# Performance work log

Hardware: AMD Instinct MI355X
Metric: run time of the kernel (lower is better)

The kernel has to match this reference:

```python
import jax, jax.numpy as jnp
import numpy as np

K_EDE = 10.0  # IR-Net EDE k
T_EDE = 0.1   # IR-Net EDE t

@jax.custom_vjp
def binquant(x):
    # forward: sign; backward: EDE STE k*t*(1 - tanh(t*x)^2)
    return jnp.sign(x)

def _bq_fwd(x):
    return jnp.sign(x), x

def _bq_bwd(x, g):
    t = jnp.tanh(x * T_EDE)
    return (K_EDE * T_EDE * (1.0 - t * t) * g,)

binquant.defvjp(_bq_fwd, _bq_bwd)

def irconv2d(x, w, stride, groups):
    # IRConv2d: per-out-channel standardize weights, sign-binarize weights
    # and activations, rescale by detached power-of-two scale, then conv.
    oc = w.shape[0]
    wf = w.reshape(oc, -1)
    mean = jnp.mean(wf, axis=-1)[:, None, None, None]
    std = jnp.std(wf, axis=-1, ddof=1)[:, None, None, None]  # torch unbiased std
    bw = (w - mean) / std
    scale = 2.0 ** jnp.round(jnp.log2(jnp.mean(jnp.abs(bw).reshape(oc, -1), axis=-1)))
    sw = jax.lax.stop_gradient(scale)[:, None, None, None]
    bw = binquant(bw) * sw
    ba = binquant(x)
    return jax.lax.conv_general_dilated(
        ba, bw, window_strides=(stride, stride), padding=((1, 1), (1, 1)),
        dimension_numbers=("NCHW", "OIHW", "NCHW"), feature_group_count=groups)

def batchnorm(x, gamma, beta, mean, var, eps=1e-5):
    inv = gamma / jnp.sqrt(var + eps)
    return x * inv[None, :, None, None] + (beta - mean * inv)[None, :, None, None]

def setup_inputs() -> dict:
    key = jax.random.key(0)
    ks = jax.random.split(key, 8)
    B, C, H, W, G = 64, 256, 28, 28, 4
    x = jax.random.normal(ks[0], (B, C, H, W), dtype=jnp.float32)
    w1 = jax.random.normal(ks[1], (G, C, C // G, 3, 3), dtype=jnp.float32) * 0.05
    g1 = jnp.ones((G, C), dtype=jnp.float32)
    b1 = jnp.zeros((G, C), dtype=jnp.float32)
    m1 = jax.random.normal(ks[2], (G, C), dtype=jnp.float32) * 0.1
    v1 = jax.random.uniform(ks[3], (G, C), dtype=jnp.float32, minval=0.5, maxval=1.5)
    w2 = jax.random.normal(ks[4], (C, C, 3, 3), dtype=jnp.float32) * 0.05
    g2 = jnp.ones((C,), dtype=jnp.float32)
    b2 = jnp.zeros((C,), dtype=jnp.float32)
    m2 = jax.random.normal(ks[5], (C,), dtype=jnp.float32) * 0.1
    v2 = jax.random.uniform(ks[6], (C,), dtype=jnp.float32, minval=0.5, maxval=1.5)
    return {"x": x, "w1": w1, "g1": g1, "b1": b1, "m1": m1, "v1": v1,
            "w2": w2, "g2": g2, "b2": b2, "m2": m2, "v2": v2}

def reference(x, w1, g1, b1, m1, v1, w2, g2, b2, m2, v2):
    groups = w1.shape[0]
    identity = x  # downsample is None
    x_max = jax.lax.stop_gradient(jnp.max(jnp.abs(x)))
    out = jnp.zeros_like(x)
    for i in range(groups):
        alpha = -1.0 + (i + 1) * 2.0 / (groups + 1)
        xi = x + alpha * x_max
        yi = irconv2d(xi, w1[i], stride=1, groups=groups)
        yi = batchnorm(yi, g1[i], b1[i], m1[i], v1[i])
        out = out + yi
    out = out + identity
    out = jnp.clip(out, -1.0, 1.0)  # Hardtanh
    identity = out
    out = irconv2d(out, w2, stride=1, groups=1)
    out = batchnorm(out, g2, b2, m2, v2)
    out = out + identity
    return jnp.clip(out, -1.0, 1.0)
```

## Files before the change

### kernel.cpp

```cpp
#include <hip/hip_runtime.h>
#include <stdint.h>

typedef uint32_t u32; typedef uint64_t u64; typedef unsigned short u16;

#define NB   64
#define NC   256
#define NG   4
#define HW   784
#define PHW  900
#define NTOT 12845056

#define OFF_XMAX 0
#define OFF_FLG1 64
#define OFF_FLG2 1088
#define OFF_W1P  2048
#define OFF_W2P  75776
#define OFF_A1   149504
#define OFF_S1   153600
#define OFF_A2   157696
#define OFF_S2   158720
#define OFF_C1   159744
#define OFF_C2   196608
#define OFF_BA1  205824
#define OFF_BZ1  7578624
#define OFF_BA2  14951424
#define OFF_BZ2  16794624

__device__ inline double wredsumd(double v) {
#pragma unroll
    for (int off = 32; off; off >>= 1) v += __shfl_xor(v, off);
    return v;
}

__global__ __launch_bounds__(256) void k_absmax(const float4* __restrict__ x, u32* __restrict__ xmax, int n4) {
    u32 m = 0;
    int idx = blockIdx.x * blockDim.x + threadIdx.x;
    int stride = gridDim.x * blockDim.x;
    for (int i = idx; i < n4; i += stride) {
        float4 v = x[i];
        m = max(m, __float_as_uint(v.x) & 0x7fffffffu);
        m = max(m, __float_as_uint(v.y) & 0x7fffffffu);
        m = max(m, __float_as_uint(v.z) & 0x7fffffffu);
        m = max(m, __float_as_uint(v.w) & 0x7fffffffu);
    }
#pragma unroll
    for (int off = 32; off; off >>= 1) {
        u32 o = (u32)__shfl_xor((int)m, off);
        m = max(m, o);
    }
    __shared__ u32 sm[4];
    int lane = threadIdx.x & 63, wid = threadIdx.x >> 6;
    if (lane == 0) sm[wid] = m;
    __syncthreads();
    if (threadIdx.x == 0) {
        u32 mm = max(max(sm[0], sm[1]), max(sm[2], sm[3]));
        atomicMax(xmax, mm);
    }
}

__global__ __launch_bounds__(256) void k_prep1(const float* __restrict__ w1, const float* __restrict__ g1,
                                               const float* __restrict__ b1, const float* __restrict__ m1,
                                               const float* __restrict__ v1, char* __restrict__ ws) {
    int lane = threadIdx.x & 63, wid = threadIdx.x >> 6;
    int cc = blockIdx.x * 4 + wid;
    int i = cc >> 8, oc = cc & 255;
    const float* wp = w1 + ((size_t)(i * 256 + oc) * 64 + lane) * 9;
    float v[9];
#pragma unroll
    for (int t = 0; t < 9; t++) v[t] = wp[t];
    double s = 0.0;
#pragma unroll
    for (int t = 0; t < 9; t++) s += (double)v[t];
    s = wredsumd(s);
    double mean = s / 576.0;
    double ssq = 0.0, sab = 0.0;
#pragma unroll
    for (int t = 0; t < 9; t++) { double d = (double)v[t] - mean; ssq += d * d; sab += fabs(d); }
    ssq = wredsumd(ssq); sab = wredsumd(sab);
    double stdv = sqrt(ssq / 575.0);
    double meanabs = sab / 576.0 / stdv;
    float scale = (float)exp2(rint(log2(meanabs)));
    int bi = i * 256 + oc;
    float inv = __fdiv_rn(g1[bi], __fsqrt_rn(__fadd_rn(v1[bi], 1e-5f)));
    float A = __fmul_rn(scale, inv);
    float S = __fsub_rn(b1[bi], __fmul_rn(m1[bi], inv));

    u64* w1p = (u64*)(ws + OFF_W1P);
    int c[9]; u64 keep = 0;
#pragma unroll
    for (int t = 0; t < 9; t++) {
        u64 bal = __ballot((double)v[t] > mean);
        c[t] = 64 - 2 * (int)__popcll(bal);
        if (lane == t) keep = bal;
    }
    if (lane < 9) w1p[(size_t)(oc * 4 + i) * 9 + lane] = keep;
    if (lane == 0) {
        ((float*)(ws + OFF_A1))[oc * 4 + i] = A;
        ((float*)(ws + OFF_S1))[oc * 4 + i] = S;
        float* C1 = (float*)(ws + OFF_C1);
#pragma unroll
        for (int pat = 0; pat < 9; pat++) {
            int rt = pat / 3, ct = pat % 3, corr = 0;
#pragma unroll
            for (int t = 0; t < 9; t++) {
                int dh = t / 3 - 1, dw = t % 3 - 1;
                bool inval = (rt == 0 && dh < 0) || (rt == 2 && dh > 0) || (ct == 0 && dw < 0) || (ct == 2 && dw > 0);
                if (inval) corr += c[t];
            }
            C1[(oc * 4 + i) * 9 + pat] = (float)(576 - corr);
        }
    }
}

__global__ __launch_bounds__(256) void k_prep2(const float* __restrict__ w2, const float* __restrict__ g2,
                                               const float* __restrict__ b2, const float* __restrict__ m2,
                                               const float* __restrict__ v2, char* __restrict__ ws) {
    int lane = threadIdx.x & 63, wid = threadIdx.x >> 6;
    int oc = blockIdx.x * 4 + wid;
    float v[36];
#pragma unroll
    for (int icw = 0; icw < 4; icw++)
#pragma unroll
        for (int t = 0; t < 9; t++)
            v[icw * 9 + t] = w2[(size_t)(oc * 256 + icw * 64 + lane) * 9 + t];
    double s = 0.0;
#pragma unroll
    for (int k = 0; k < 36; k++) s += (double)v[k];
    s = wredsumd(s);
    double mean = s / 2304.0;
    double ssq = 0.0, sab = 0.0;
#pragma unroll
    for (int k = 0; k < 36; k++) { double d = (double)v[k] - mean; ssq += d * d; sab += fabs(d); }
    ssq = wredsumd(ssq); sab = wredsumd(sab);
    double stdv = sqrt(ssq / 2303.0);
    double meanabs = sab / 2304.0 / stdv;
    float scale = (float)exp2(rint(log2(meanabs)));
    float inv = __fdiv_rn(g2[oc], __fsqrt_rn(__fadd_rn(v2[oc], 1e-5f)));
    float A = __fmul_rn(scale, inv);
    float S = __fsub_rn(b2[oc], __fmul_rn(m2[oc], inv));

    u64* w2p = (u64*)(ws + OFF_W2P);
    int c2[9] = {0,0,0,0,0,0,0,0,0};
    u64 keep = 0;
#pragma unroll
    for (int icw = 0; icw < 4; icw++)
#pragma unroll
        for (int t = 0; t < 9; t++) {
            u64 bal = __ballot((double)v[icw * 9 + t] > mean);
            c2[t] += 64 - 2 * (int)__popcll(bal);
            if (lane == t * 4 + icw) keep = bal;
        }
    if (lane < 36) w2p[(size_t)oc * 36 + lane] = keep;
    if (lane == 0) {
        ((float*)(ws + OFF_A2))[oc] = A;
        ((float*)(ws + OFF_S2))[oc] = S;
        float* C2 = (float*)(ws + OFF_C2);
#pragma unroll
        for (int pat = 0; pat < 9; pat++) {
            int rt = pat / 3, ct = pat % 3, corr = 0;
#pragma unroll
            for (int t = 0; t < 9; t++) {
                int dh = t / 3 - 1, dw = t % 3 - 1;
                bool inval = (rt == 0 && dh < 0) || (rt == 2 && dh > 0) || (ct == 0 && dw < 0) || (ct == 2 && dw > 0);
                if (inval) corr += c2[t];
            }
            C2[oc * 9 + pat] = (float)(2304 - corr);
        }
    }
}

__global__ __launch_bounds__(256) void k_pack(const float* __restrict__ x, char* __restrict__ ws) {
    int g = blockIdx.x / 225, bb = blockIdx.x % 225;
    int fp = bb * 256 + threadIdx.x;
    int n = fp / 900, idx = fp - n * 900;
    int ph = idx / 30, pw = idx - ph * 30;
    u64* ba1 = (u64*)(ws + OFF_BA1);
    u64* bz1 = (u64*)(ws + OFF_BZ1);
    bool halo = (ph == 0) | (ph == 29) | (pw == 0) | (pw == 29);
    if (halo) {
#pragma unroll
        for (int i = 0; i < 4; i++) {
            size_t o = (size_t)((i * 64 + n) * 4 + g) * 900 + idx;
            ba1[o] = 0; bz1[o] = 0;
        }
        ((u64*)(ws + OFF_BA2))[(size_t)(n * 4 + g) * 900 + idx] = 0;
        ((u64*)(ws + OFF_BZ2))[(size_t)(n * 4 + g) * 900 + idx] = 0;
        return;
    }
    float xmax = *(const float*)(ws + OFF_XMAX);
    float t0 = __fmul_rn(-0.6f, xmax), t1 = __fmul_rn(-0.2f, xmax);
    float t2 = __fmul_rn(0.2f, xmax), t3 = __fmul_rn(0.6f, xmax);
    int h = ph - 1, w = pw - 1;
    const float* xb = x + (size_t)(n * 256 + g * 64) * 784 + (h * 28 + w);
    u64 wd0 = 0, wd1 = 0, wd2 = 0, wd3 = 0;
    u64 zd0 = 0, zd1 = 0, zd2 = 0, zd3 = 0;
#pragma unroll 8
    for (int c = 0; c < 64; c++) {
        float v = xb[(size_t)c * 784];
        float s0 = __fadd_rn(v, t0), s1 = __fadd_rn(v, t1);
        float s2 = __fadd_rn(v, t2), s3 = __fadd_rn(v, t3);
        wd0 |= (u64)(s0 > 0.f) << c;  zd0 |= (u64)(s0 == 0.f) << c;
        wd1 |= (u64)(s1 > 0.f) << c;  zd1 |= (u64)(s1 == 0.f) << c;
        wd2 |= (u64)(s2 > 0.f) << c;  zd2 |= (u64)(s2 == 0.f) << c;
        wd3 |= (u64)(s3 > 0.f) << c;  zd3 |= (u64)(s3 == 0.f) << c;
    }
    ba1[(size_t)((0 * 64 + n) * 4 + g) * 900 + idx] = wd0;
    ba1[(size_t)((1 * 64 + n) * 4 + g) * 900 + idx] = wd1;
    ba1[(size_t)((2 * 64 + n) * 4 + g) * 900 + idx] = wd2;
    ba1[(size_t)((3 * 64 + n) * 4 + g) * 900 + idx] = wd3;
    bz1[(size_t)((0 * 64 + n) * 4 + g) * 900 + idx] = zd0;
    bz1[(size_t)((1 * 64 + n) * 4 + g) * 900 + idx] = zd1;
    bz1[(size_t)((2 * 64 + n) * 4 + g) * 900 + idx] = zd2;
    bz1[(size_t)((3 * 64 + n) * 4 + g) * 900 + idx] = zd3;
    if (zd0 | zd1 | zd2 | zd3) atomicOr((u32*)(ws + OFF_FLG1) + (n * 4 + g), 1u);
}

__global__ __launch_bounds__(256) void k_conv1(const float* __restrict__ x, float* __restrict__ out,
                                               char* __restrict__ ws) {
    int gq = blockIdx.x / 196, bb = blockIdx.x % 196;
    int g = gq >> 2, q = gq & 3;
    int fp = bb * 256 + threadIdx.x;
    int n = fp / 784, pos = fp - n * 784;
    int h = pos / 28, w = pos - h * 28;
    int rt = (h == 0) ? 0 : ((h == 27) ? 2 : 1);
    int ct = (w == 0) ? 0 : ((w == 27) ? 2 : 1);
    int pat = rt * 3 + ct;
    int pb = (h + 1) * 30 + (w + 1);

    __shared__ u64   wsm[576];
    __shared__ float c1s[576];
    {
        const u64* wsrc = (const u64*)(ws + OFF_W1P) + (size_t)g * 2304 + q * 576;
        const float* C1 = (const float*)(ws + OFF_C1) + g * 2304 + q * 576;
        for (int k = threadIdx.x; k < 576; k += 256) { wsm[k] = wsrc[k]; c1s[k] = C1[k]; }
    }
    const u64* ba1 = (const u64*)(ws + OFF_BA1);
    u64 aw[4][9];
#pragma unroll
    for (int i = 0; i < 4; i++) {
        const u64* bp = ba1 + (size_t)((i * 64 + n) * 4 + g) * 900 + pb;
#pragma unroll
        for (int t = 0; t < 9; t++) { int dh = t / 3 - 1, dw = t % 3 - 1; aw[i][t] = bp[dh * 30 + dw]; }
    }
    u32 zflag = ((const u32*)(ws + OFF_FLG1))[n * 4 + g];
    __syncthreads();

    const float* A1 = (const float*)(ws + OFF_A1) + g * 256 + q * 64;
    const float* S1 = (const float*)(ws + OFF_S1) + g * 256 + q * 64;
    const float* xb = x + (size_t)(n * 256 + g * 64 + q * 16) * 784 + pos;
    float* ob = out + (size_t)(n * 256 + g * 64 + q * 16) * 784 + pos;
    u32 bits = 0, zbits = 0;
    if (!zflag) {
        float id[16];
#pragma unroll
        for (int j = 0; j < 16; j++) id[j] = xb[(size_t)j * 784];
#pragma unroll
        for (int j = 0; j < 16; j++) {
            const u64* wp = wsm + j * 36;
            u32 D[4];
#pragma unroll
            for (int i = 0; i < 4; i++) {
                u32 d = 0;
#pragma unroll
                for (int t = 0; t < 9; t++) d += (u32)__popcll(aw[i][t] ^ wp[i * 9 + t]);
                D[i] = d;
            }
            float acc = 0.f;
#pragma unroll
            for (int i = 0; i < 4; i++) {
                float cf = c1s[(j * 4 + i) * 9 + pat];
                float conv = __fmaf_rn(-2.f, (float)D[i], cf);
                float yi = __fadd_rn(__fmul_rn(conv, A1[j * 4 + i]), S1[j * 4 + i]);
                acc = (i == 0) ? yi : __fadd_rn(acc, yi);
            }
            float o = __fadd_rn(acc, id[j]);
            o = fminf(fmaxf(o, -1.f), 1.f);
            bits  |= (u32)(o > 0.f) << j;
            zbits |= (u32)(o == 0.f) << j;
            ob[(size_t)j * 784] = o;
        }
    } else {
        const u64* bz1 = (const u64*)(ws + OFF_BZ1);
        for (int j = 0; j < 16; j++) {
            const u64* wp = wsm + j * 36;
            float acc = 0.f;
#pragma unroll
            for (int i = 0; i < 4; i++) {
                const u64* zp = bz1 + (size_t)((i * 64 + n) * 4 + g) * 900 + pb;
                u32 d = 0; int cz = 0;
#pragma unroll
                for (int t = 0; t < 9; t++) {
                    int dh = t / 3 - 1, dw = t % 3 - 1;
                    u64 zt = zp[dh * 30 + dw];
                    d += (u32)__popcll(aw[i][t] ^ wp[i * 9 + t]);
                    cz += 2 * (int)__popcll(zt & wp[i * 9 + t]) - (int)__popcll(zt);
                }
                float cf = c1s[(j * 4 + i) * 9 + pat];
                float conv = __fadd_rn(__fmaf_rn(-2.f, (float)d, cf), (float)cz);
                float yi = __fadd_rn(__fmul_rn(conv, A1[j * 4 + i]), S1[j * 4 + i]);
                acc = (i == 0) ? yi : __fadd_rn(acc, yi);
            }
            float o = __fadd_rn(acc, xb[(size_t)j * 784]);
            o = fminf(fmaxf(o, -1.f), 1.f);
            bits  |= (u32)(o > 0.f) << j;
            zbits |= (u32)(o == 0.f) << j;
            ob[(size_t)j * 784] = o;
        }
    }
    size_t widx = (size_t)(n * 4 + g) * 900 + pb;
    ((u16*)(ws + OFF_BA2))[widx * 4 + q] = (u16)bits;
    ((u16*)(ws + OFF_BZ2))[widx * 4 + q] = (u16)zbits;
    if (zbits) atomicOr((u32*)(ws + OFF_FLG2) + n, 1u);
}

__global__ __launch_bounds__(256) void k_conv2(float* __restrict__ out, char* __restrict__ ws) {
    int tq = blockIdx.x / 196, bb = blockIdx.x % 196;
    int oq = tq >> 2, q = tq & 3;
    int fp = bb * 256 + threadIdx.x;
    int n = fp / 784, pos = fp - n * 784;
    int h = pos / 28, w = pos - h * 28;
    int rt = (h == 0) ? 0 : ((h == 27) ? 2 : 1);
    int ct = (w == 0) ? 0 : ((w == 27) ? 2 : 1);
    int pat = rt * 3 + ct;
    int pb = (h + 1) * 30 + (w + 1);

    __shared__ u64   wsm[576];
    __shared__ float c2s[144];
    {
        const u64* wsrc = (const u64*)(ws + OFF_W2P) + (size_t)(oq * 64 + q * 16) * 36;
        for (int k = threadIdx.x; k < 576; k += 256) wsm[k] = wsrc[k];
        const float* C2 = (const float*)(ws + OFF_C2) + (oq * 64 + q * 16) * 9;
        if (threadIdx.x < 144) c2s[threadIdx.x] = C2[threadIdx.x];
    }
    const u64* ba2 = (const u64*)(ws + OFF_BA2);
    u64 aw[4][9];
#pragma unroll
    for (int icw = 0; icw < 4; icw++) {
        const u64* bp = ba2 + (size_t)(n * 4 + icw) * 900 + pb;
#pragma unroll
        for (int t = 0; t < 9; t++) { int dh = t / 3 - 1, dw = t % 3 - 1; aw[icw][t] = bp[dh * 30 + dw]; }
    }
    u32 zflag = ((const u32*)(ws + OFF_FLG2))[n];
    __syncthreads();

    const float* A2 = (const float*)(ws + OFF_A2) + oq * 64 + q * 16;
    const float* S2 = (const float*)(ws + OFF_S2) + oq * 64 + q * 16;
    float* ob = out + ((size_t)n * 256 + oq * 64 + q * 16) * 784 + pos;
    if (!zflag) {
        float id[16];
#pragma unroll
        for (int j = 0; j < 16; j++) id[j] = ob[(size_t)j * 784];
#pragma unroll
        for (int j = 0; j < 16; j++) {
            const u64* wp = wsm + j * 36;
            u32 dp0 = 0, dp1 = 0, dp2 = 0, dp3 = 0;
#pragma unroll
            for (int t = 0; t < 9; t++) {
                dp0 += (u32)__popcll(aw[0][t] ^ wp[t * 4 + 0]);
                dp1 += (u32)__popcll(aw[1][t] ^ wp[t * 4 + 1]);
                dp2 += (u32)__popcll(aw[2][t] ^ wp[t * 4 + 2]);
                dp3 += (u32)__popcll(aw[3][t] ^ wp[t * 4 + 3]);
            }
            u32 d = (dp0 + dp1) + (dp2 + dp3);
            float cf = c2s[j * 9 + pat];
            float conv = __fmaf_rn(-2.f, (float)d, cf);
            float y = __fadd_rn(__fmul_rn(conv, A2[j]), S2[j]);
            float o = __fadd_rn(y, id[j]);
            o = fminf(fmaxf(o, -1.f), 1.f);
            ob[(size_t)j * 784] = o;
        }
    } else {
        const u64* bz2 = (const u64*)(ws + OFF_BZ2);
        for (int j = 0; j < 16; j++) {
            const u64* wp = wsm + j * 36;
            u32 d = 0; int cz = 0;
#pragma unroll
            for (int icw = 0; icw < 4; icw++) {
                const u64* zp = bz2 + (size_t)(n * 4 + icw) * 900 + pb;
#pragma unroll
                for (int t = 0; t < 9; t++) {
                    int dh = t / 3 - 1, dw = t % 3 - 1;
                    u64 zt = zp[dh * 30 + dw];
                    d += (u32)__popcll(aw[icw][t] ^ wp[t * 4 + icw]);
                    cz += 2 * (int)__popcll(zt & wp[t * 4 + icw]) - (int)__popcll(zt);
                }
            }
            float cf = c2s[j * 9 + pat];
            float conv = __fadd_rn(__fmaf_rn(-2.f, (float)d, cf), (float)cz);
            float y = __fadd_rn(__fmul_rn(conv, A2[j]), S2[j]);
            float idf = ob[(size_t)j * 784];
            float o = __fadd_rn(y, idf);
            o = fminf(fmaxf(o, -1.f), 1.f);
            ob[(size_t)j * 784] = o;
        }
    }
}

extern "C" void kernel_launch(void* const* d_in, const int* in_sizes, int n_in,
                              void* d_out, int out_size, void* d_ws, size_t ws_size,
                              hipStream_t stream) {
    const float* x  = (const float*)d_in[0];
    const float* w1 = (const float*)d_in[1];
    const float* g1 = (const float*)d_in[2];
    const float* b1 = (const float*)d_in[3];
    const float* m1 = (const float*)d_in[4];
    const float* v1 = (const float*)d_in[5];
    const float* w2 = (const float*)d_in[6];
    const float* g2 = (const float*)d_in[7];
    const float* b2 = (const float*)d_in[8];
    const float* m2 = (const float*)d_in[9];
    const float* v2 = (const float*)d_in[10];
    float* out = (float*)d_out;
    char* ws = (char*)d_ws;

    hipMemsetAsync(ws, 0, 2048, stream);
    k_absmax<<<512, 256, 0, stream>>>((const float4*)x, (u32*)(ws + OFF_XMAX), NTOT / 4);
    k_prep1<<<256, 256, 0, stream>>>(w1, g1, b1, m1, v1, ws);
    k_prep2<<<64, 256, 0, stream>>>(w2, g2, b2, m2, v2, ws);
    k_pack<<<900, 256, 0, stream>>>(x, ws);
    k_conv1<<<3136, 256, 0, stream>>>(x, out, ws);
    k_conv2<<<3136, 256, 0, stream>>>(out, ws);
}
```

Measured before the change: 322.4 us.

## Replace popcount binary convs with FP8 MFMA implicit-GEMM path

Adds a new path that encodes the sign-binarized weights and activations as FP8 values (+1/-1/0) in MFMA-friendly tiled layouts and runs both convolutions as implicit GEMMs with 32x32x16 fp8 MFMA instructions. Zero padding is a literal halo of zeros, so the per-pattern border correction tables and zero-flag branches are no longer needed. The path runs only when the workspace is large enough, and falls back to the old XOR/popcount kernels otherwise. It uses a much larger workspace (byte-per-element activations) and depends on the FP8 accumulation giving exact integer sums.

```diff
diff --git a/kernel.cpp b/kernel.cpp
--- a/kernel.cpp
+++ b/kernel.cpp
@@ -2,12 +2,9 @@
 #include <stdint.h>
 
 typedef uint32_t u32; typedef uint64_t u64; typedef unsigned short u16;
-
-#define NB   64
-#define NC   256
-#define NG   4
-#define HW   784
-#define PHW  900
+typedef long long i64;
+typedef float v16f __attribute__((ext_vector_type(16)));
+
 #define NTOT 12845056
 
 #define OFF_XMAX 0
@@ -26,6 +23,14 @@
 #define OFF_BA2  14951424
 #define OFF_BZ2  16794624
 
+#define MOFF_AS1   64
+#define MOFF_AS2   8256
+#define MOFF_W1F   16384
+#define MOFF_W2F   606208
+#define MOFF_ACT1  1196032
+#define MOFF_ACT2  60182528
+#define MNEED      74940416ULL
+
 __device__ inline double wredsumd(double v) {
 #pragma unroll
     for (int off = 32; off; off >>= 1) v += __shfl_xor(v, off);
@@ -58,9 +63,10 @@
     }
 }
 
-__global__ __launch_bounds__(256) void k_prep1(const float* __restrict__ w1, const float* __restrict__ g1,
-                                               const float* __restrict__ b1, const float* __restrict__ m1,
-                                               const float* __restrict__ v1, char* __restrict__ ws) {
+
+__global__ __launch_bounds__(256) void k_prep1m(const float* __restrict__ w1, const float* __restrict__ g1,
+                                                const float* __restrict__ b1, const float* __restrict__ m1,
+                                                const float* __restrict__ v1, char* __restrict__ ws) {
     int lane = threadIdx.x & 63, wid = threadIdx.x >> 6;
     int cc = blockIdx.x * 4 + wid;
     int i = cc >> 8, oc = cc & 255;
@@ -85,36 +91,25 @@
     float A = __fmul_rn(scale, inv);
     float S = __fsub_rn(b1[bi], __fmul_rn(m1[bi], inv));
 
-    u64* w1p = (u64*)(ws + OFF_W1P);
-    int c[9]; u64 keep = 0;
+    unsigned char* w1f = (unsigned char*)(ws + MOFF_W1F);
+    int g = oc >> 6, oc64 = oc & 63, ocb = oc64 >> 5, oc32 = oc64 & 31;
+    size_t blk0 = ((size_t)(((g * 4 + i) * 2 + ocb) * 18)) << 10;
 #pragma unroll
     for (int t = 0; t < 9; t++) {
-        u64 bal = __ballot((double)v[t] > mean);
-        c[t] = 64 - 2 * (int)__popcll(bal);
-        if (lane == t) keep = bal;
-    }
-    if (lane < 9) w1p[(size_t)(oc * 4 + i) * 9 + lane] = keep;
-    if (lane == 0) {
-        ((float*)(ws + OFF_A1))[oc * 4 + i] = A;
-        ((float*)(ws + OFF_S1))[oc * 4 + i] = S;
-        float* C1 = (float*)(ws + OFF_C1);
-#pragma unroll
-        for (int pat = 0; pat < 9; pat++) {
-            int rt = pat / 3, ct = pat % 3, corr = 0;
-#pragma unroll
-            for (int t = 0; t < 9; t++) {
-                int dh = t / 3 - 1, dw = t % 3 - 1;
-                bool inval = (rt == 0 && dh < 0) || (rt == 2 && dh > 0) || (ct == 0 && dw < 0) || (ct == 2 && dw > 0);
-                if (inval) corr += c[t];
-            }
-            C1[(oc * 4 + i) * 9 + pat] = (float)(576 - corr);
-        }
-    }
-}
-
-__global__ __launch_bounds__(256) void k_prep2(const float* __restrict__ w2, const float* __restrict__ g2,
-                                               const float* __restrict__ b2, const float* __restrict__ m2,
-                                               const float* __restrict__ v2, char* __restrict__ ws) {
+        int k = t * 64 + lane;
+        int kb = k >> 4;
+        size_t off = blk0 + ((size_t)(kb >> 1) << 10)
+                   + (size_t)((((k >> 3) & 1) * 32 + oc32) * 16 + (kb & 1) * 8 + (k & 7));
+        double dv = (double)v[t];
+        w1f[off] = (dv > mean) ? 0x38 : ((dv < mean) ? 0xB8 : 0x00);
+    }
+    if (lane == 0)
+        ((float2*)(ws + MOFF_AS1))[(g * 4 + i) * 64 + oc64] = make_float2(A, S);
+}
+
+__global__ __launch_bounds__(256) void k_prep2m(const float* __restrict__ w2, const float* __restrict__ g2,
+                                                const float* __restrict__ b2, const float* __restrict__ m2,
+                                                const float* __restrict__ v2, char* __restrict__ ws) {
     int lane = threadIdx.x & 63, wid = threadIdx.x >> 6;
     int oc = blockIdx.x * 4 + wid;
     float v[36];
@@ -139,6 +134,257 @@
     float A = __fmul_rn(scale, inv);
     float S = __fsub_rn(b2[oc], __fmul_rn(m2[oc], inv));
 
+    unsigned char* w2f = (unsigned char*)(ws + MOFF_W2F);
+    int ocb = oc >> 5, oc32 = oc & 31;
+#pragma unroll
+    for (int icw = 0; icw < 4; icw++)
+#pragma unroll
+        for (int t = 0; t < 9; t++) {
+            int ic = icw * 64 + lane;
+            int k = t * 256 + ic;
+            int kb = k >> 4;
+            size_t off = ((size_t)(ocb * 72 + (kb >> 1)) << 10)
+                       + (size_t)((((ic >> 3) & 1) * 32 + oc32) * 16 + (kb & 1) * 8 + (ic & 7));
+            double dv = (double)v[icw * 9 + t];
+            w2f[off] = (dv > mean) ? 0x38 : ((dv < mean) ? 0xB8 : 0x00);
+        }
+    if (lane == 0)
+        ((float2*)(ws + MOFF_AS2))[oc] = make_float2(A, S);
+}
+
+__global__ __launch_bounds__(256) void k_packm(const float* __restrict__ x, char* __restrict__ ws) {
+    int fp = blockIdx.x * 256 + threadIdx.x;
+    int q = fp & 3; int rr = fp >> 2;
+    int idx = rr % 900; int ng = rr / 900;
+    int g = ng & 3, n = ng >> 2;
+    char* act1 = ws + MOFF_ACT1;
+    char* act2 = ws + MOFF_ACT2;
+    int ph = idx / 30, pw = idx - ph * 30;
+    bool halo = (ph == 0) | (ph == 29) | (pw == 0) | (pw == 29);
+    if (halo) {
+        int4 z = make_int4(0, 0, 0, 0);
+#pragma unroll
+        for (int i = 0; i < 4; i++)
+            *(int4*)(act1 + (((size_t)((i * 64 + n) * 4 + g) * 900 + idx) << 6) + q * 16) = z;
+        *(int4*)(act2 + (((size_t)(n * 900 + idx)) << 8) + g * 64 + q * 16) = z;
+        return;
+    }
+    float xmax = *(const float*)(ws);
+    float t0 = __fmul_rn(-0.6f, xmax), t1 = __fmul_rn(-0.2f, xmax);
+    float t2 = __fmul_rn(0.2f, xmax), t3 = __fmul_rn(0.6f, xmax);
+    const float* xb = x + (size_t)(n * 256 + g * 64 + q * 16) * 784 + ((ph - 1) * 28 + (pw - 1));
+    u32 w0[4] = {0,0,0,0}, w1_[4] = {0,0,0,0}, w2_[4] = {0,0,0,0}, w3_[4] = {0,0,0,0};
+#pragma unroll
+    for (int c = 0; c < 16; c++) {
+        float vv = xb[(size_t)c * 784];
+        int sh = (c & 3) * 8, wi = c >> 2;
+        float s0 = __fadd_rn(vv, t0), s1 = __fadd_rn(vv, t1);
+        float s2 = __fadd_rn(vv, t2), s3 = __fadd_rn(vv, t3);
+        w0[wi] |= (s0 > 0.f ? 0x38u : (s0 == 0.f ? 0u : 0xB8u)) << sh;
+        w1_[wi] |= (s1 > 0.f ? 0x38u : (s1 == 0.f ? 0u : 0xB8u)) << sh;
+        w2_[wi] |= (s2 > 0.f ? 0x38u : (s2 == 0.f ? 0u : 0xB8u)) << sh;
+        w3_[wi] |= (s3 > 0.f ? 0x38u : (s3 == 0.f ? 0u : 0xB8u)) << sh;
+    }
+    size_t rb = ((size_t)(n * 4 + g) * 900 + idx) << 6;
+    size_t istr = (size_t)256 * 900 * 64;
+    *(int4*)(act1 + rb + 0 * istr + q * 16) = make_int4(w0[0], w0[1], w0[2], w0[3]);
+    *(int4*)(act1 + rb + 1 * istr + q * 16) = make_int4(w1_[0], w1_[1], w1_[2], w1_[3]);
+    *(int4*)(act1 + rb + 2 * istr + q * 16) = make_int4(w2_[0], w2_[1], w2_[2], w2_[3]);
+    *(int4*)(act1 + rb + 3 * istr + q * 16) = make_int4(w3_[0], w3_[1], w3_[2], w3_[3]);
+}
+
+__global__ __launch_bounds__(256) void k_conv1m(const float* __restrict__ x, float* __restrict__ out,
+                                                char* __restrict__ ws) {
+    const int dofs[9] = {-31, -30, -29, -1, 0, 1, 29, 30, 31};
+    int wv = blockIdx.x * 4 + (threadIdx.x >> 6);
+    int l = threadIdx.x & 63, l31 = l & 31, lh = l >> 5;
+    int ocb = wv & 1; int r1 = wv >> 1;
+    int pt = r1 % 25; int ng = r1 / 25;
+    int g = ng & 3, n = ng >> 2;
+    int pos = pt * 32 + l31;
+    int h = pos / 28, ww = pos - h * 28;
+    int pb = (h + 1) * 30 + (ww + 1);
+    const char* act1 = ws + MOFF_ACT1;
+    const char* w1f = ws + MOFF_W1F;
+    const char* bbase[4];
+    const char* abase[4];
+#pragma unroll
+    for (int i = 0; i < 4; i++) {
+        bbase[i] = act1 + (((size_t)((i * 64 + n) * 4 + g) * 900 + pb) << 6) + lh * 8;
+        abase[i] = w1f + (((size_t)(((g * 4 + i) * 2 + ocb) * 18)) << 10) + l * 16;
+    }
+    v16f acc[4];
+#pragma unroll
+    for (int i = 0; i < 4; i++)
+#pragma unroll
+        for (int e = 0; e < 16; e++) acc[i][e] = 0.f;
+#pragma unroll
+    for (int kb2 = 0; kb2 < 18; kb2++) {
+        int D = dofs[kb2 >> 1] * 64 + (kb2 & 1) * 32;
+#pragma unroll
+        for (int i = 0; i < 4; i++) {
+            const char* wp = abase[i] + (kb2 << 10);
+            i64 alo = *(const i64*)(wp);
+            i64 ahi = *(const i64*)(wp + 8);
+            i64 blo = *(const i64*)(bbase[i] + D);
+            i64 bhi = *(const i64*)(bbase[i] + D + 16);
+            acc[i] = __builtin_amdgcn_mfma_f32_32x32x16_fp8_fp8(alo, blo, acc[i], 0, 0, 0);
+            acc[i] = __builtin_amdgcn_mfma_f32_32x32x16_fp8_fp8(ahi, bhi, acc[i], 0, 0, 0);
+        }
+    }
+    bool valid = pos < 784;
+    const float2* AS1 = (const float2*)(ws + MOFF_AS1);
+    char* act2 = ws + MOFF_ACT2;
+#pragma unroll
+    for (int r = 0; r < 16; r++) {
+        int oct = (r & 3) + 8 * (r >> 2) + 4 * lh;
+        int c = g * 64 + ocb * 32 + oct;
+        float accf = 0.f;
+#pragma unroll
+        for (int i = 0; i < 4; i++) {
+            float2 as = AS1[(g * 4 + i) * 64 + ocb * 32 + oct];
+            float yi = __fadd_rn(__fmul_rn(acc[i][r], as.x), as.y);
+            accf = (i == 0) ? yi : __fadd_rn(accf, yi);
+        }
+        if (valid) {
+            size_t oo = ((size_t)(n * 256 + c)) * 784 + pos;
+            float o = __fadd_rn(accf, x[oo]);
+            o = fminf(fmaxf(o, -1.f), 1.f);
+            out[oo] = o;
+            unsigned char s8 = (o > 0.f) ? 0x38 : ((o == 0.f) ? 0x00 : 0xB8);
+            act2[((size_t)(n * 900 + pb)) * 256 + c] = s8;
+        }
+    }
+}
+
+__global__ __launch_bounds__(256) void k_conv2m(float* __restrict__ out, char* __restrict__ ws) {
+    const int dofs[9] = {-31, -30, -29, -1, 0, 1, 29, 30, 31};
+    int wv = blockIdx.x * 4 + (threadIdx.x >> 6);
+    int l = threadIdx.x & 63, l31 = l & 31, lh = l >> 5;
+    int ocb = wv & 7; int r2 = wv >> 3;
+    int pt = r2 % 25; int n = r2 / 25;
+    int pos = pt * 32 + l31;
+    int h = pos / 28, ww = pos - h * 28;
+    int pb = (h + 1) * 30 + (ww + 1);
+    const char* bbase = ws + MOFF_ACT2 + (((size_t)(n * 900 + pb)) << 8) + lh * 8;
+    const char* abase = ws + MOFF_W2F + (((size_t)(ocb * 72)) << 10) + l * 16;
+    v16f accP, accQ;
+#pragma unroll
+    for (int e = 0; e < 16; e++) { accP[e] = 0.f; accQ[e] = 0.f; }
+#pragma unroll
+    for (int kb2 = 0; kb2 < 72; kb2++) {
+        const char* wp = abase + (kb2 << 10);
+        i64 alo = *(const i64*)(wp);
+        i64 ahi = *(const i64*)(wp + 8);
+        int D = dofs[kb2 >> 3] * 256 + (kb2 & 7) * 32;
+        i64 blo = *(const i64*)(bbase + D);
+        i64 bhi = *(const i64*)(bbase + D + 16);
+        if (kb2 & 1) {
+            accQ = __builtin_amdgcn_mfma_f32_32x32x16_fp8_fp8(alo, blo, accQ, 0, 0, 0);
+            accQ = __builtin_amdgcn_mfma_f32_32x32x16_fp8_fp8(ahi, bhi, accQ, 0, 0, 0);
+        } else {
+            accP = __builtin_amdgcn_mfma_f32_32x32x16_fp8_fp8(alo, blo, accP, 0, 0, 0);
+            accP = __builtin_amdgcn_mfma_f32_32x32x16_fp8_fp8(ahi, bhi, accP, 0, 0, 0);
+        }
+    }
+    bool valid = pos < 784;
+    const float2* AS2 = (const float2*)(ws + MOFF_AS2);
+#pragma unroll
+    for (int r = 0; r < 16; r++) {
+        int oct = (r & 3) + 8 * (r >> 2) + 4 * lh;
+        int c = ocb * 32 + oct;
+        float conv = __fadd_rn(accP[r], accQ[r]);
+        float2 as = AS2[c];
+        float y = __fadd_rn(__fmul_rn(conv, as.x), as.y);
+        if (valid) {
+            size_t oo = ((size_t)(n * 256 + c)) * 784 + pos;
+            float o = __fadd_rn(y, out[oo]);
+            o = fminf(fmaxf(o, -1.f), 1.f);
+            out[oo] = o;
+        }
+    }
+}
+
+
+__global__ __launch_bounds__(256) void k_prep1(const float* __restrict__ w1, const float* __restrict__ g1,
+                                               const float* __restrict__ b1, const float* __restrict__ m1,
+                                               const float* __restrict__ v1, char* __restrict__ ws) {
+    int lane = threadIdx.x & 63, wid = threadIdx.x >> 6;
+    int cc = blockIdx.x * 4 + wid;
+    int i = cc >> 8, oc = cc & 255;
+    const float* wp = w1 + ((size_t)(i * 256 + oc) * 64 + lane) * 9;
+    float v[9];
+#pragma unroll
+    for (int t = 0; t < 9; t++) v[t] = wp[t];
+    double s = 0.0;
+#pragma unroll
+    for (int t = 0; t < 9; t++) s += (double)v[t];
+    s = wredsumd(s);
+    double mean = s / 576.0;
+    double ssq = 0.0, sab = 0.0;
+#pragma unroll
+    for (int t = 0; t < 9; t++) { double d = (double)v[t] - mean; ssq += d * d; sab += fabs(d); }
+    ssq = wredsumd(ssq); sab = wredsumd(sab);
+    double stdv = sqrt(ssq / 575.0);
+    double meanabs = sab / 576.0 / stdv;
+    float scale = (float)exp2(rint(log2(meanabs)));
+    int bi = i * 256 + oc;
+    float inv = __fdiv_rn(g1[bi], __fsqrt_rn(__fadd_rn(v1[bi], 1e-5f)));
+    float A = __fmul_rn(scale, inv);
+    float S = __fsub_rn(b1[bi], __fmul_rn(m1[bi], inv));
+    u64* w1p = (u64*)(ws + OFF_W1P);
+    int c[9]; u64 keep = 0;
+#pragma unroll
+    for (int t = 0; t < 9; t++) {
+        u64 bal = __ballot((double)v[t] > mean);
+        c[t] = 64 - 2 * (int)__popcll(bal);
+        if (lane == t) keep = bal;
+    }
+    if (lane < 9) w1p[(size_t)(oc * 4 + i) * 9 + lane] = keep;
+    if (lane == 0) {
+        ((float*)(ws + OFF_A1))[oc * 4 + i] = A;
+        ((float*)(ws + OFF_S1))[oc * 4 + i] = S;
+        float* C1 = (float*)(ws + OFF_C1);
+#pragma unroll
+        for (int pat = 0; pat < 9; pat++) {
+            int rt = pat / 3, ct = pat % 3, corr = 0;
+#pragma unroll
+            for (int t = 0; t < 9; t++) {
+                int dh = t / 3 - 1, dw = t % 3 - 1;
+                bool inval = (rt == 0 && dh < 0) || (rt == 2 && dh > 0) || (ct == 0 && dw < 0) || (ct == 2 && dw > 0);
+                if (inval) corr += c[t];
+            }
+            C1[(oc * 4 + i) * 9 + pat] = (float)(576 - corr);
+        }
+    }
+}
+
+__global__ __launch_bounds__(256) void k_prep2(const float* __restrict__ w2, const float* __restrict__ g2,
+                                               const float* __restrict__ b2, const float* __restrict__ m2,
+                                               const float* __restrict__ v2, char* __restrict__ ws) {
+    int lane = threadIdx.x & 63, wid = threadIdx.x >> 6;
+    int oc = blockIdx.x * 4 + wid;
+    float v[36];
+#pragma unroll
+    for (int icw = 0; icw < 4; icw++)
+#pragma unroll
+        for (int t = 0; t < 9; t++)
+            v[icw * 9 + t] = w2[(size_t)(oc * 256 + icw * 64 + lane) * 9 + t];
+    double s = 0.0;
+#pragma unroll
+    for (int k = 0; k < 36; k++) s += (double)v[k];
+    s = wredsumd(s);
+    double mean = s / 2304.0;
+    double ssq = 0.0, sab = 0.0;
+#pragma unroll
+    for (int k = 0; k < 36; k++) { double d = (double)v[k] - mean; ssq += d * d; sab += fabs(d); }
+    ssq = wredsumd(ssq); sab = wredsumd(sab);
+    double stdv = sqrt(ssq / 2303.0);
+    double meanabs = sab / 2304.0 / stdv;
+    float scale = (float)exp2(rint(log2(meanabs)));
+    float inv = __fdiv_rn(g2[oc], __fsqrt_rn(__fadd_rn(v2[oc], 1e-5f)));
+    float A = __fmul_rn(scale, inv);
+    float S = __fsub_rn(b2[oc], __fmul_rn(m2[oc], inv));
     u64* w2p = (u64*)(ws + OFF_W2P);
     int c2[9] = {0,0,0,0,0,0,0,0,0};
     u64 keep = 0;
@@ -226,7 +472,6 @@
     int ct = (w == 0) ? 0 : ((w == 27) ? 2 : 1);
     int pat = rt * 3 + ct;
     int pb = (h + 1) * 30 + (w + 1);
-
     __shared__ u64   wsm[576];
     __shared__ float c1s[576];
     {
@@ -244,7 +489,6 @@
     }
     u32 zflag = ((const u32*)(ws + OFF_FLG1))[n * 4 + g];
     __syncthreads();
-
     const float* A1 = (const float*)(ws + OFF_A1) + g * 256 + q * 64;
     const float* S1 = (const float*)(ws + OFF_S1) + g * 256 + q * 64;
     const float* xb = x + (size_t)(n * 256 + g * 64 + q * 16) * 784 + pos;
@@ -323,7 +567,6 @@
     int ct = (w == 0) ? 0 : ((w == 27) ? 2 : 1);
     int pat = rt * 3 + ct;
     int pb = (h + 1) * 30 + (w + 1);
-
     __shared__ u64   wsm[576];
     __shared__ float c2s[144];
     {
@@ -342,7 +585,6 @@
     }
     u32 zflag = ((const u32*)(ws + OFF_FLG2))[n];
     __syncthreads();
-
     const float* A2 = (const float*)(ws + OFF_A2) + oq * 64 + q * 16;
     const float* S2 = (const float*)(ws + OFF_S2) + oq * 64 + q * 16;
     float* ob = out + ((size_t)n * 256 + oq * 64 + q * 16) * 784 + pos;
@@ -413,11 +655,20 @@
     float* out = (float*)d_out;
     char* ws = (char*)d_ws;
 
+    bool mf = (ws_size >= MNEED);
     hipMemsetAsync(ws, 0, 2048, stream);
-    k_absmax<<<512, 256, 0, stream>>>((const float4*)x, (u32*)(ws + OFF_XMAX), NTOT / 4);
-    k_prep1<<<256, 256, 0, stream>>>(w1, g1, b1, m1, v1, ws);
-    k_prep2<<<64, 256, 0, stream>>>(w2, g2, b2, m2, v2, ws);
-    k_pack<<<900, 256, 0, stream>>>(x, ws);
-    k_conv1<<<3136, 256, 0, stream>>>(x, out, ws);
-    k_conv2<<<3136, 256, 0, stream>>>(out, ws);
-}
+    k_absmax<<<512, 256, 0, stream>>>((const float4*)x, (u32*)ws, NTOT / 4);
+    if (mf) {
+        k_prep1m<<<256, 256, 0, stream>>>(w1, g1, b1, m1, v1, ws);
+        k_prep2m<<<64, 256, 0, stream>>>(w2, g2, b2, m2, v2, ws);
+        k_packm<<<3600, 256, 0, stream>>>(x, ws);
+        k_conv1m<<<3200, 256, 0, stream>>>(x, out, ws);
+        k_conv2m<<<3200, 256, 0, stream>>>(out, ws);
+    } else {
+        k_prep1<<<256, 256, 0, stream>>>(w1, g1, b1, m1, v1, ws);
+        k_prep2<<<64, 256, 0, stream>>>(w2, g2, b2, m2, v2, ws);
+        k_pack<<<900, 256, 0, stream>>>(x, ws);
+        k_conv1<<<3136, 256, 0, stream>>>(x, out, ws);
+        k_conv2<<<3136, 256, 0, stream>>>(out, ws);
+    }
+}
```

Measured after the change: 616.6 us. 1.91x slower.
